# Kernel optimization log

Hardware: AMD Instinct MI355X
Metric: run time of the kernel (lower is better)

Reference implementation:

```python
import jax, jax.numpy as jnp
import numpy as np

EPS = 1.1920929e-07  # torch RMSNorm default eps = finfo(float32).eps
B, S, H, HQ, HKV, D, I, E, TOPK = 2, 512, 1024, 16, 4, 64, 4096, 8, 2


def rmsnorm(x, w):
    return x * jax.lax.rsqrt(jnp.mean(x * x, axis=-1, keepdims=True) + EPS) * w


def setup_inputs() -> dict:
    key = jax.random.key(0)
    ks = jax.random.split(key, 24)

    def w(k, shape, fan_in):
        return jax.random.normal(k, shape, jnp.float32) / np.float32(np.sqrt(fan_in))

    return {
        "x": jax.random.normal(ks[0], (B, S, H), jnp.float32),
        "norm1_w": jnp.ones((H,), jnp.float32),
        "q_w": w(ks[1], (H, HQ * D), H), "q_b": jnp.zeros((HQ * D,), jnp.float32),
        "k_w": w(ks[2], (H, HKV * D), H), "k_b": jnp.zeros((HKV * D,), jnp.float32),
        "v_w": w(ks[3], (H, HKV * D), H), "v_b": jnp.zeros((HKV * D,), jnp.float32),
        "o_w": w(ks[4], (HQ * D, H), HQ * D), "o_b": jnp.zeros((H,), jnp.float32),
        "norm2_w": jnp.ones((H,), jnp.float32),
        "router_w": w(ks[5], (H, E), H), "router_b": jnp.zeros((E,), jnp.float32),
        "gate_w": w(ks[6], (E, H, I), H), "gate_b": jnp.zeros((E, I), jnp.float32),
        "up_w": w(ks[7], (E, H, I), H), "up_b": jnp.zeros((E, I), jnp.float32),
        "down_w": w(ks[8], (E, I, H), I), "down_b": jnp.zeros((E, H), jnp.float32),
    }


def reference(x, norm1_w, q_w, q_b, k_w, k_b, v_w, v_b, o_w, o_b, norm2_w,
              router_w, router_b, gate_w, gate_b, up_w, up_b, down_w, down_b):
    # ---- self-attention (GQA, no mask, dropout=0) ----
    h = rmsnorm(x, norm1_w)
    q = (h @ q_w + q_b).reshape(B, S, HQ, D).transpose(0, 2, 1, 3)   # [B,HQ,S,D]
    k = (h @ k_w + k_b).reshape(B, S, HKV, D).transpose(0, 2, 1, 3)  # [B,HKV,S,D]
    v = (h @ v_w + v_b).reshape(B, S, HKV, D).transpose(0, 2, 1, 3)
    g = HQ // HKV
    k = jnp.repeat(k, g, axis=1)  # repeat_interleave, matches SDPA enable_gqa
    v = jnp.repeat(v, g, axis=1)
    scores = jnp.einsum('bhqd,bhkd->bhqk', q, k) * np.float32(1.0 / np.sqrt(D))
    attn = jax.nn.softmax(scores, axis=-1)
    o = jnp.einsum('bhqk,bhkd->bhqd', attn, v).transpose(0, 2, 1, 3).reshape(B, S, HQ * D)
    x = x + (o @ o_w + o_b)

    # ---- MoE (top-k routing, softmax over top-k logits) ----
    t = rmsnorm(x, norm2_w).reshape(B * S, H)                # [T,H]
    logits = t @ router_w + router_b                         # [T,E]
    top_v, top_i = jax.lax.top_k(logits, TOPK)
    probs = jax.nn.softmax(top_v, axis=-1)                   # [T,K]
    combine = jnp.einsum('tke,tk->te', jax.nn.one_hot(top_i, E, dtype=t.dtype), probs)  # [T,E]
    gt = jnp.einsum('th,ehi->tei', t, gate_w) + gate_b       # [T,E,I]
    up = jnp.einsum('th,ehi->tei', t, up_w) + up_b
    dn = jnp.einsum('tei,eih->teh', jax.nn.silu(gt) * up, down_w) + down_b  # [T,E,H]
    moe = jnp.einsum('teh,te->th', dn, combine).reshape(B, S, H)
    return moe + x
```

## Files before the change

kernel.cpp:

```cpp
#include <hip/hip_runtime.h>
#include <math.h>

#define T 1024
#define H 1024
#define S 512
#define BB 2
#define HQ 16
#define HKV 4
#define DH 64
#define NI 4096
#define NE 8
#define EPSR 1.1920929e-07f

typedef unsigned short u16;
using short8 = __attribute__((ext_vector_type(8))) short;
using f32x4  = __attribute__((ext_vector_type(4))) float;
using float4v = __attribute__((ext_vector_type(4))) float;

__device__ __forceinline__ float bf2f(u16 u) {
    unsigned int x = ((unsigned int)u) << 16;
    return __uint_as_float(x);
}
__device__ __forceinline__ u16 f2bf(float f) {
    unsigned int x = __float_as_uint(f);
    return (u16)((x + 0x7fffu + ((x >> 16) & 1u)) >> 16);
}

__global__ __launch_bounds__(256) void rmsnorm_k(const float* __restrict__ xin,
                                                 const float* __restrict__ w,
                                                 u16* __restrict__ out) {
    int t = blockIdx.x;
    int tid = threadIdx.x;
    float vals[4];
    float ss = 0.f;
#pragma unroll
    for (int i = 0; i < 4; i++) {
        int c = tid + i * 256;
        float v = xin[(long)t * H + c];
        vals[i] = v;
        ss += v * v;
    }
    int lane = tid & 63, wid = tid >> 6;
#pragma unroll
    for (int o = 32; o; o >>= 1) ss += __shfl_xor(ss, o);
    __shared__ float red[4];
    __shared__ float rtot;
    if (lane == 0) red[wid] = ss;
    __syncthreads();
    if (tid == 0) {
        float s = red[0] + red[1] + red[2] + red[3];
        rtot = rsqrtf(s / (float)H + EPSR);
    }
    __syncthreads();
    float r = rtot;
#pragma unroll
    for (int i = 0; i < 4; i++) {
        int c = tid + i * 256;
        out[(long)t * H + c] = f2bf(vals[i] * r * w[c]);
    }
}

template <int MODE>
__global__ __launch_bounds__(256) void gemm64(
    const u16* __restrict__ A, int lda,
    const float* __restrict__ B0, const float* __restrict__ B1, int ldb,
    const float* __restrict__ bias0, const float* __restrict__ bias1,
    const float* __restrict__ resid,
    void* __restrict__ out,
    int M, int N, int K,
    const int* __restrict__ ecnt, const int* __restrict__ eoff,
    const int* __restrict__ tlist, const float* __restrict__ tscale,
    u16* __restrict__ act, float* __restrict__ moe) {
    int e = blockIdx.z;
    int row0 = blockIdx.y * 64;
    int n0 = blockIdx.x * 64;
    int cnt = M, loff = 0;
    if (MODE >= 3) {
        cnt = ecnt[e];
        loff = eoff[e];
        if (row0 >= cnt) return;
        B0 += (long)e * (long)K * (long)ldb;
        bias0 += (long)e * N;
        if (MODE == 3) {
            B1 += (long)e * (long)K * (long)ldb;
            bias1 += (long)e * N;
        }
    }

    const int tid = threadIdx.x, lane = tid & 63, wv = tid >> 6;
    const int wm = wv >> 1, wc = wv & 1;

    __shared__ u16 As[64][40];
    __shared__ u16 Bs0[4][64][8];
    __shared__ u16 Bs1[(MODE == 3) ? 4 : 1][64][8];

    f32x4 acc0[2][2] = {};
    f32x4 acc1[2][2] = {};

    int arow = tid >> 2;
    int acol = (tid & 3) * 8;
    long arow_g;
    if (MODE == 3) {
        int r = row0 + arow;
        if (r >= cnt) r = cnt - 1;
        arow_g = tlist[loff + r];
    } else if (MODE == 4) {
        int r = row0 + arow;
        if (r >= cnt) r = cnt - 1;
        arow_g = loff + r;
    } else {
        arow_g = row0 + arow;
    }
    const u16* Aptr = A + arow_g * (long)lda + acol;

    int brow = tid >> 3;
    int bcol = (tid & 7) * 8;
    const float* B0ptr = B0 + (long)brow * ldb + n0 + bcol;
    const float* B1ptr = (MODE == 3) ? (B1 + (long)brow * ldb + n0 + bcol) : nullptr;

    for (int k0 = 0; k0 < K; k0 += 32) {
        short8 av = *(const short8*)(Aptr + k0);
        *(short8*)&As[arow][acol] = av;
        {
            float4v b0a = *(const float4v*)(B0ptr + (long)k0 * ldb);
            float4v b0b = *(const float4v*)(B0ptr + (long)k0 * ldb + 4);
#pragma unroll
            for (int u = 0; u < 4; u++) Bs0[brow >> 3][bcol + u][brow & 7] = f2bf(b0a[u]);
#pragma unroll
            for (int u = 0; u < 4; u++) Bs0[brow >> 3][bcol + 4 + u][brow & 7] = f2bf(b0b[u]);
        }
        if (MODE == 3) {
            float4v b1a = *(const float4v*)(B1ptr + (long)k0 * ldb);
            float4v b1b = *(const float4v*)(B1ptr + (long)k0 * ldb + 4);
#pragma unroll
            for (int u = 0; u < 4; u++) Bs1[brow >> 3][bcol + u][brow & 7] = f2bf(b1a[u]);
#pragma unroll
            for (int u = 0; u < 4; u++) Bs1[brow >> 3][bcol + 4 + u][brow & 7] = f2bf(b1b[u]);
        }
        __syncthreads();
        int quad = lane >> 4;
#pragma unroll
        for (int mi = 0; mi < 2; mi++) {
            int m = wm * 32 + mi * 16 + (lane & 15);
            short8 af = *(const short8*)&As[m][quad * 8];
#pragma unroll
            for (int ni = 0; ni < 2; ni++) {
                int n = wc * 32 + ni * 16 + (lane & 15);
                short8 bfr = *(const short8*)&Bs0[quad][n][0];
                acc0[mi][ni] = __builtin_amdgcn_mfma_f32_16x16x32_bf16(af, bfr, acc0[mi][ni], 0, 0, 0);
                if (MODE == 3) {
                    short8 bfu = *(const short8*)&Bs1[quad][n][0];
                    acc1[mi][ni] = __builtin_amdgcn_mfma_f32_16x16x32_bf16(af, bfu, acc1[mi][ni], 0, 0, 0);
                }
            }
        }
        __syncthreads();
    }

#pragma unroll
    for (int mi = 0; mi < 2; mi++) {
#pragma unroll
        for (int ni = 0; ni < 2; ni++) {
            int rbase = wm * 32 + mi * 16 + ((lane >> 4) << 2);
            int col = wc * 32 + ni * 16 + (lane & 15);
            int gcol = n0 + col;
#pragma unroll
            for (int r = 0; r < 4; r++) {
                int row = rbase + r;
                float v = acc0[mi][ni][r];
                if (MODE == 1) {
                    ((u16*)out)[(long)(row0 + row) * N + gcol] = f2bf(v + bias0[gcol]);
                } else if (MODE == 2) {
                    long idx = (long)(row0 + row) * N + gcol;
                    ((float*)out)[idx] = v + bias0[gcol] + resid[idx];
                } else if (MODE == 3) {
                    int rr = row0 + row;
                    if (rr < cnt) {
                        float g = v + bias0[gcol];
                        float u2 = acc1[mi][ni][r] + bias1[gcol];
                        float sg = g / (1.f + __expf(-g));
                        act[(long)(loff + rr) * NI + gcol] = f2bf(sg * u2);
                    }
                } else if (MODE == 4) {
                    int rr = row0 + row;
                    if (rr < cnt) {
                        int tok = tlist[loff + rr];
                        float sc = tscale[loff + rr];
                        atomicAdd(&moe[(long)tok * H + gcol], sc * (v + bias0[gcol]));
                    }
                }
            }
        }
    }
}

__global__ __launch_bounds__(256) void attn_k(const u16* __restrict__ q,
                                              const u16* __restrict__ k,
                                              const u16* __restrict__ v,
                                              u16* __restrict__ o) {
    int tid = threadIdx.x, lane = tid & 63, wv = tid >> 6;
    int w = blockIdx.x * 4 + wv;
    int sq = w % S;
    int h = (w / S) % HQ;
    int b = w / (S * HQ);
    int hk = h >> 2;
    int tq = b * S + sq;
    __shared__ float qs[4][64];
    __shared__ float ps[4][512];
    float* Q = qs[wv];
    float* P = ps[wv];
    Q[lane] = bf2f(q[(long)tq * (HQ * DH) + h * DH + lane]) * 0.125f;
    __syncthreads();
    float sc[8];
    float m = -1e30f;
#pragma unroll
    for (int jj = 0; jj < 8; jj++) {
        int j = lane + jj * 64;
        const u16* kr = k + (long)(b * S + j) * (HKV * DH) + hk * DH;
        float a = 0.f;
#pragma unroll
        for (int c = 0; c < 8; c++) {
            short8 kv8 = *(const short8*)(kr + c * 8);
#pragma unroll
            for (int u = 0; u < 8; u++) a += Q[c * 8 + u] * bf2f((u16)kv8[u]);
        }
        sc[jj] = a;
        m = fmaxf(m, a);
    }
#pragma unroll
    for (int o2 = 32; o2; o2 >>= 1) m = fmaxf(m, __shfl_xor(m, o2));
    float l = 0.f;
#pragma unroll
    for (int jj = 0; jj < 8; jj++) {
        float p = __expf(sc[jj] - m);
        P[lane + jj * 64] = p;
        l += p;
    }
#pragma unroll
    for (int o2 = 32; o2; o2 >>= 1) l += __shfl_xor(l, o2);
    __syncthreads();
    float inv = 1.f / l;
    float acc = 0.f;
    const u16* vb = v + (long)(b * S) * (HKV * DH) + hk * DH + lane;
#pragma unroll 4
    for (int j = 0; j < 512; j++) acc += P[j] * bf2f(vb[(long)j * (HKV * DH)]);
    o[(long)tq * (HQ * DH) + h * DH + lane] = f2bf(acc * inv);
}

__global__ __launch_bounds__(256) void router_k(const u16* __restrict__ t2,
                                                const float* __restrict__ rw,
                                                const float* __restrict__ rb,
                                                int* __restrict__ topi,
                                                float* __restrict__ probs) {
    int tid = threadIdx.x, lane = tid & 63, wv = tid >> 6;
    int tok = blockIdx.x * 4 + wv;
    float acc[NE] = {0.f, 0.f, 0.f, 0.f, 0.f, 0.f, 0.f, 0.f};
    for (int i = lane; i < H; i += 64) {
        float tv = bf2f(t2[(long)tok * H + i]);
        const float* r = rw + (long)i * NE;
        float4v ra = *(const float4v*)r;
        float4v rbv = *(const float4v*)(r + 4);
#pragma unroll
        for (int e = 0; e < 4; e++) acc[e] += tv * ra[e];
#pragma unroll
        for (int e = 0; e < 4; e++) acc[4 + e] += tv * rbv[e];
    }
#pragma unroll
    for (int e = 0; e < NE; e++)
#pragma unroll
        for (int o = 32; o; o >>= 1) acc[e] += __shfl_xor(acc[e], o);
    if (lane == 0) {
        float lg[NE];
#pragma unroll
        for (int e = 0; e < NE; e++) lg[e] = acc[e] + rb[e];
        int i0 = 0;
        float v0 = lg[0];
#pragma unroll
        for (int e = 1; e < NE; e++)
            if (lg[e] > v0) { v0 = lg[e]; i0 = e; }
        int i1 = -1;
        float v1 = -1e30f;
#pragma unroll
        for (int e = 0; e < NE; e++) {
            if (e == i0) continue;
            if (lg[e] > v1) { v1 = lg[e]; i1 = e; }
        }
        float ex = __expf(v1 - v0);
        float p0 = 1.f / (1.f + ex);
        topi[tok * 2] = i0;
        topi[tok * 2 + 1] = i1;
        probs[tok * 2] = p0;
        probs[tok * 2 + 1] = ex * p0;
    }
}

__global__ void build_k(const int* __restrict__ topi, const float* __restrict__ probs,
                        int* __restrict__ gcnt, int* __restrict__ goff,
                        int* __restrict__ list, float* __restrict__ lscale) {
    __shared__ int cnt[NE], off[NE], fill[NE];
    int t = threadIdx.x;
    if (t < NE) cnt[t] = 0;
    __syncthreads();
    int e0 = topi[2 * t], e1 = topi[2 * t + 1];
    atomicAdd(&cnt[e0], 1);
    atomicAdd(&cnt[e1], 1);
    __syncthreads();
    if (t == 0) {
        int run = 0;
        for (int e = 0; e < NE; e++) {
            off[e] = run;
            fill[e] = run;
            run += cnt[e];
        }
    }
    __syncthreads();
    if (t < NE) {
        gcnt[t] = cnt[t];
        goff[t] = off[t];
    }
    int p0 = atomicAdd(&fill[e0], 1);
    list[p0] = t;
    lscale[p0] = probs[2 * t];
    int p1 = atomicAdd(&fill[e1], 1);
    list[p1] = t;
    lscale[p1] = probs[2 * t + 1];
}

__global__ void zero_k(float* __restrict__ p, int n) {
    int i = blockIdx.x * 256 + threadIdx.x;
    if (i < n) p[i] = 0.f;
}

__global__ void final_k(const float* __restrict__ x1, const float* __restrict__ moe,
                        float* __restrict__ out) {
    int i = blockIdx.x * 256 + threadIdx.x;
    out[i] = x1[i] + moe[i];
}

extern "C" void kernel_launch(void* const* d_in, const int* in_sizes, int n_in,
                              void* d_out, int out_size, void* d_ws, size_t ws_size,
                              hipStream_t stream) {
    const float* x = (const float*)d_in[0];
    const float* norm1_w = (const float*)d_in[1];
    const float* q_w = (const float*)d_in[2];
    const float* q_b = (const float*)d_in[3];
    const float* k_w = (const float*)d_in[4];
    const float* k_b = (const float*)d_in[5];
    const float* v_w = (const float*)d_in[6];
    const float* v_b = (const float*)d_in[7];
    const float* o_w = (const float*)d_in[8];
    const float* o_b = (const float*)d_in[9];
    const float* norm2_w = (const float*)d_in[10];
    const float* router_w = (const float*)d_in[11];
    const float* router_b = (const float*)d_in[12];
    const float* gate_w = (const float*)d_in[13];
    const float* gate_b = (const float*)d_in[14];
    const float* up_w = (const float*)d_in[15];
    const float* up_b = (const float*)d_in[16];
    const float* down_w = (const float*)d_in[17];
    const float* down_b = (const float*)d_in[18];

    char* w = (char*)d_ws;
    u16* h1 = (u16*)w;            w += (long)T * H * 2;
    u16* qb = (u16*)w;            w += (long)T * (HQ * DH) * 2;
    u16* kb = (u16*)w;            w += (long)T * (HKV * DH) * 2;
    u16* vb = (u16*)w;            w += (long)T * (HKV * DH) * 2;
    u16* ao = (u16*)w;            w += (long)T * (HQ * DH) * 2;
    float* x1 = (float*)w;        w += (long)T * H * 4;
    u16* t2 = (u16*)w;            w += (long)T * H * 2;
    int* topi = (int*)w;          w += T * 2 * 4;
    float* probs = (float*)w;     w += T * 2 * 4;
    int* gcnt = (int*)w;          w += 64;
    int* goff = (int*)w;          w += 64;
    int* list = (int*)w;          w += 2048 * 4;
    float* lscale = (float*)w;    w += 2048 * 4;
    u16* act = (u16*)w;           w += (long)2112 * NI * 2;
    float* moe = (float*)w;       w += (long)T * H * 4;

    rmsnorm_k<<<T, 256, 0, stream>>>(x, norm1_w, h1);
    gemm64<1><<<dim3(16, 16, 1), 256, 0, stream>>>(h1, 1024, q_w, nullptr, 1024, q_b, nullptr,
                                                   nullptr, qb, 1024, 1024, 1024,
                                                   nullptr, nullptr, nullptr, nullptr, nullptr, nullptr);
    gemm64<1><<<dim3(4, 16, 1), 256, 0, stream>>>(h1, 1024, k_w, nullptr, 256, k_b, nullptr,
                                                  nullptr, kb, 1024, 256, 1024,
                                                  nullptr, nullptr, nullptr, nullptr, nullptr, nullptr);
    gemm64<1><<<dim3(4, 16, 1), 256, 0, stream>>>(h1, 1024, v_w, nullptr, 256, v_b, nullptr,
                                                  nullptr, vb, 1024, 256, 1024,
                                                  nullptr, nullptr, nullptr, nullptr, nullptr, nullptr);
    attn_k<<<(BB * HQ * S) / 4, 256, 0, stream>>>(qb, kb, vb, ao);
    gemm64<2><<<dim3(16, 16, 1), 256, 0, stream>>>(ao, 1024, o_w, nullptr, 1024, o_b, nullptr,
                                                   x, x1, 1024, 1024, 1024,
                                                   nullptr, nullptr, nullptr, nullptr, nullptr, nullptr);
    rmsnorm_k<<<T, 256, 0, stream>>>(x1, norm2_w, t2);
    router_k<<<T / 4, 256, 0, stream>>>(t2, router_w, router_b, topi, probs);
    build_k<<<1, 1024, 0, stream>>>(topi, probs, gcnt, goff, list, lscale);
    zero_k<<<(T * H) / 256, 256, 0, stream>>>(moe, T * H);
    gemm64<3><<<dim3(NI / 64, 16, NE), 256, 0, stream>>>(t2, 1024, gate_w, up_w, NI,
                                                         gate_b, up_b, nullptr, nullptr,
                                                         0, NI, 1024,
                                                         gcnt, goff, list, lscale, act, nullptr);
    gemm64<4><<<dim3(H / 64, 16, NE), 256, 0, stream>>>(act, NI, down_w, nullptr, H,
                                                        down_b, nullptr, nullptr, nullptr,
                                                        0, H, NI,
                                                        gcnt, goff, list, lscale, nullptr, moe);
    final_k<<<(T * H) / 256, 256, 0, stream>>>(x1, moe, (float*)d_out);
}
```

Measured before the change: 1.164 ms.

## Pre-transpose weights to bf16, enlarge GEMM tiles to 128, fuse QKV projection

Every weight matrix is first transposed and converted to bf16 by a dedicated kernel. The GEMM then loads K-contiguous bf16 rows with vector loads instead of converting fp32 inside the inner loop. GEMM tiles grow from 64x64 to 128x128 with a 4x4 MFMA block per wave, and the Q/K/V projections merge into one GEMM that writes a packed QKV buffer read by attention. The transposes run inside the timed call and rewrite about 200MB of expert weights on every call. The larger tiles also leave fewer blocks for the small routed expert batches.

```diff
diff --git a/kernel.cpp b/kernel.cpp
--- a/kernel.cpp
+++ b/kernel.cpp
@@ -26,6 +26,34 @@
     return (u16)((x + 0x7fffu + ((x >> 16) & 1u)) >> 16);
 }
 
+__global__ __launch_bounds__(256) void transpose_k(const float* __restrict__ W,
+                                                   u16* __restrict__ WT,
+                                                   int K, int N,
+                                                   long in_bs, long out_bs) {
+    int z = blockIdx.z;
+    W += z * in_bs;
+    WT += z * out_bs;
+    int n0 = blockIdx.x * 64, k0 = blockIdx.y * 64;
+    __shared__ u16 tile[64][68];
+    int t = threadIdx.x;
+    int r = t >> 4, c = (t & 15) * 4;
+#pragma unroll
+    for (int p = 0; p < 4; p++) {
+        float4v v = *(const float4v*)(W + (long)(k0 + r + p * 16) * N + n0 + c);
+#pragma unroll
+        for (int u = 0; u < 4; u++) tile[r + p * 16][c + u] = f2bf(v[u]);
+    }
+    __syncthreads();
+    int n = t >> 3, k8 = (t & 7) * 8;
+#pragma unroll
+    for (int p = 0; p < 2; p++) {
+        short8 o;
+#pragma unroll
+        for (int j = 0; j < 8; j++) o[j] = (short)tile[k8 + j][n + p * 32];
+        *(short8*)(WT + (long)(n0 + n + p * 32) * K + k0 + k8) = o;
+    }
+}
+
 __global__ __launch_bounds__(256) void rmsnorm_k(const float* __restrict__ xin,
                                                  const float* __restrict__ w,
                                                  u16* __restrict__ out) {
@@ -61,9 +89,9 @@
 }
 
 template <int MODE>
-__global__ __launch_bounds__(256) void gemm64(
+__global__ __launch_bounds__(256) void gemm128(
     const u16* __restrict__ A, int lda,
-    const float* __restrict__ B0, const float* __restrict__ B1, int ldb,
+    const u16* __restrict__ BT0, const u16* __restrict__ BT1,
     const float* __restrict__ bias0, const float* __restrict__ bias1,
     const float* __restrict__ resid,
     void* __restrict__ out,
@@ -72,98 +100,97 @@
     const int* __restrict__ tlist, const float* __restrict__ tscale,
     u16* __restrict__ act, float* __restrict__ moe) {
     int e = blockIdx.z;
-    int row0 = blockIdx.y * 64;
-    int n0 = blockIdx.x * 64;
+    int row0 = blockIdx.y * 128;
+    int n0 = blockIdx.x * 128;
     int cnt = M, loff = 0;
     if (MODE >= 3) {
         cnt = ecnt[e];
         loff = eoff[e];
         if (row0 >= cnt) return;
-        B0 += (long)e * (long)K * (long)ldb;
+        BT0 += (long)e * (long)K * (long)NI * ((MODE == 3) ? 1 : 0) + ((MODE == 4) ? (long)e * (long)K * (long)H : 0);
         bias0 += (long)e * N;
         if (MODE == 3) {
-            B1 += (long)e * (long)K * (long)ldb;
+            BT1 += (long)e * (long)K * (long)NI;
             bias1 += (long)e * N;
         }
     }
 
     const int tid = threadIdx.x, lane = tid & 63, wv = tid >> 6;
-    const int wm = wv >> 1, wc = wv & 1;
-
-    __shared__ u16 As[64][40];
-    __shared__ u16 Bs0[4][64][8];
-    __shared__ u16 Bs1[(MODE == 3) ? 4 : 1][64][8];
-
-    f32x4 acc0[2][2] = {};
-    f32x4 acc1[2][2] = {};
-
-    int arow = tid >> 2;
-    int acol = (tid & 3) * 8;
-    long arow_g;
-    if (MODE == 3) {
-        int r = row0 + arow;
-        if (r >= cnt) r = cnt - 1;
-        arow_g = tlist[loff + r];
-    } else if (MODE == 4) {
-        int r = row0 + arow;
-        if (r >= cnt) r = cnt - 1;
-        arow_g = loff + r;
-    } else {
-        arow_g = row0 + arow;
-    }
-    const u16* Aptr = A + arow_g * (long)lda + acol;
-
-    int brow = tid >> 3;
-    int bcol = (tid & 7) * 8;
-    const float* B0ptr = B0 + (long)brow * ldb + n0 + bcol;
-    const float* B1ptr = (MODE == 3) ? (B1 + (long)brow * ldb + n0 + bcol) : nullptr;
+    const int wm = wv >> 1, wn = wv & 1;
+    const int quad = lane >> 4, lm = lane & 15;
+
+    __shared__ u16 As[128][32];
+    __shared__ u16 Bs0[128][32];
+    __shared__ u16 Bs1[(MODE == 3) ? 128 : 1][32];
+
+    f32x4 acc0[4][4] = {};
+    f32x4 acc1[(MODE == 3) ? 4 : 1][4] = {};
+
+    int sa_row = tid >> 2;
+    int sa_k = (tid & 3) * 8;
+    long arow_g[2];
+#pragma unroll
+    for (int p = 0; p < 2; p++) {
+        int r = row0 + sa_row + p * 64;
+        if (MODE == 3) {
+            if (r >= cnt) r = row0 + ((cnt - 1 - row0) > 0 ? (cnt - 1 - row0) : 0);
+            int rr = (row0 + sa_row + p * 64 < cnt) ? (row0 + sa_row + p * 64) : (cnt - 1);
+            arow_g[p] = tlist[loff + rr];
+        } else if (MODE == 4) {
+            int rr = (r < cnt) ? r : (cnt - 1);
+            arow_g[p] = loff + rr;
+        } else {
+            arow_g[p] = r;
+        }
+    }
+    const u16* Ap0 = A + arow_g[0] * (long)lda + sa_k;
+    const u16* Ap1 = A + arow_g[1] * (long)lda + sa_k;
+    const u16* Bp0 = BT0 + (long)(n0 + sa_row) * K + sa_k;
+    const u16* Bp1 = BT0 + (long)(n0 + sa_row + 64) * K + sa_k;
+    const u16* Cp0 = (MODE == 3) ? (BT1 + (long)(n0 + sa_row) * K + sa_k) : nullptr;
+    const u16* Cp1 = (MODE == 3) ? (BT1 + (long)(n0 + sa_row + 64) * K + sa_k) : nullptr;
 
     for (int k0 = 0; k0 < K; k0 += 32) {
-        short8 av = *(const short8*)(Aptr + k0);
-        *(short8*)&As[arow][acol] = av;
-        {
-            float4v b0a = *(const float4v*)(B0ptr + (long)k0 * ldb);
-            float4v b0b = *(const float4v*)(B0ptr + (long)k0 * ldb + 4);
-#pragma unroll
-            for (int u = 0; u < 4; u++) Bs0[brow >> 3][bcol + u][brow & 7] = f2bf(b0a[u]);
-#pragma unroll
-            for (int u = 0; u < 4; u++) Bs0[brow >> 3][bcol + 4 + u][brow & 7] = f2bf(b0b[u]);
-        }
+        short8 a0 = *(const short8*)(Ap0 + k0);
+        short8 a1 = *(const short8*)(Ap1 + k0);
+        short8 b0 = *(const short8*)(Bp0 + k0);
+        short8 b1 = *(const short8*)(Bp1 + k0);
+        short8 c0, c1;
         if (MODE == 3) {
-            float4v b1a = *(const float4v*)(B1ptr + (long)k0 * ldb);
-            float4v b1b = *(const float4v*)(B1ptr + (long)k0 * ldb + 4);
-#pragma unroll
-            for (int u = 0; u < 4; u++) Bs1[brow >> 3][bcol + u][brow & 7] = f2bf(b1a[u]);
-#pragma unroll
-            for (int u = 0; u < 4; u++) Bs1[brow >> 3][bcol + 4 + u][brow & 7] = f2bf(b1b[u]);
+            c0 = *(const short8*)(Cp0 + k0);
+            c1 = *(const short8*)(Cp1 + k0);
         }
         __syncthreads();
-        int quad = lane >> 4;
-#pragma unroll
-        for (int mi = 0; mi < 2; mi++) {
-            int m = wm * 32 + mi * 16 + (lane & 15);
-            short8 af = *(const short8*)&As[m][quad * 8];
-#pragma unroll
-            for (int ni = 0; ni < 2; ni++) {
-                int n = wc * 32 + ni * 16 + (lane & 15);
-                short8 bfr = *(const short8*)&Bs0[quad][n][0];
-                acc0[mi][ni] = __builtin_amdgcn_mfma_f32_16x16x32_bf16(af, bfr, acc0[mi][ni], 0, 0, 0);
+        *(short8*)&As[sa_row][sa_k] = a0;
+        *(short8*)&As[sa_row + 64][sa_k] = a1;
+        *(short8*)&Bs0[sa_row][sa_k] = b0;
+        *(short8*)&Bs0[sa_row + 64][sa_k] = b1;
+        if (MODE == 3) {
+            *(short8*)&Bs1[sa_row][sa_k] = c0;
+            *(short8*)&Bs1[sa_row + 64][sa_k] = c1;
+        }
+        __syncthreads();
+#pragma unroll
+        for (int mi = 0; mi < 4; mi++) {
+            short8 af = *(const short8*)&As[wm * 64 + mi * 16 + lm][quad * 8];
+#pragma unroll
+            for (int ni = 0; ni < 4; ni++) {
+                short8 bf = *(const short8*)&Bs0[wn * 64 + ni * 16 + lm][quad * 8];
+                acc0[mi][ni] = __builtin_amdgcn_mfma_f32_16x16x32_bf16(af, bf, acc0[mi][ni], 0, 0, 0);
                 if (MODE == 3) {
-                    short8 bfu = *(const short8*)&Bs1[quad][n][0];
-                    acc1[mi][ni] = __builtin_amdgcn_mfma_f32_16x16x32_bf16(af, bfu, acc1[mi][ni], 0, 0, 0);
+                    short8 cf = *(const short8*)&Bs1[wn * 64 + ni * 16 + lm][quad * 8];
+                    acc1[mi][ni] = __builtin_amdgcn_mfma_f32_16x16x32_bf16(af, cf, acc1[mi][ni], 0, 0, 0);
                 }
             }
         }
-        __syncthreads();
-    }
-
-#pragma unroll
-    for (int mi = 0; mi < 2; mi++) {
-#pragma unroll
-        for (int ni = 0; ni < 2; ni++) {
-            int rbase = wm * 32 + mi * 16 + ((lane >> 4) << 2);
-            int col = wc * 32 + ni * 16 + (lane & 15);
-            int gcol = n0 + col;
+    }
+
+#pragma unroll
+    for (int mi = 0; mi < 4; mi++) {
+#pragma unroll
+        for (int ni = 0; ni < 4; ni++) {
+            int rbase = wm * 64 + mi * 16 + quad * 4;
+            int gcol = n0 + wn * 64 + ni * 16 + lm;
 #pragma unroll
             for (int r = 0; r < 4; r++) {
                 int row = rbase + r;
@@ -194,9 +221,8 @@
     }
 }
 
-__global__ __launch_bounds__(256) void attn_k(const u16* __restrict__ q,
-                                              const u16* __restrict__ k,
-                                              const u16* __restrict__ v,
+#define QKVLD 1536
+__global__ __launch_bounds__(256) void attn_k(const u16* __restrict__ qkv,
                                               u16* __restrict__ o) {
     int tid = threadIdx.x, lane = tid & 63, wv = tid >> 6;
     int w = blockIdx.x * 4 + wv;
@@ -209,14 +235,14 @@
     __shared__ float ps[4][512];
     float* Q = qs[wv];
     float* P = ps[wv];
-    Q[lane] = bf2f(q[(long)tq * (HQ * DH) + h * DH + lane]) * 0.125f;
+    Q[lane] = bf2f(qkv[(long)tq * QKVLD + h * DH + lane]) * 0.125f;
     __syncthreads();
     float sc[8];
     float m = -1e30f;
 #pragma unroll
     for (int jj = 0; jj < 8; jj++) {
         int j = lane + jj * 64;
-        const u16* kr = k + (long)(b * S + j) * (HKV * DH) + hk * DH;
+        const u16* kr = qkv + (long)(b * S + j) * QKVLD + 1024 + hk * DH;
         float a = 0.f;
 #pragma unroll
         for (int c = 0; c < 8; c++) {
@@ -241,9 +267,9 @@
     __syncthreads();
     float inv = 1.f / l;
     float acc = 0.f;
-    const u16* vb = v + (long)(b * S) * (HKV * DH) + hk * DH + lane;
+    const u16* vb = qkv + (long)(b * S) * QKVLD + 1280 + hk * DH + lane;
 #pragma unroll 4
-    for (int j = 0; j < 512; j++) acc += P[j] * bf2f(vb[(long)j * (HKV * DH)]);
+    for (int j = 0; j < 512; j++) acc += P[j] * bf2f(vb[(long)j * QKVLD]);
     o[(long)tq * (HQ * DH) + h * DH + lane] = f2bf(acc * inv);
 }
 
@@ -324,6 +350,15 @@
     int p1 = atomicAdd(&fill[e1], 1);
     list[p1] = t;
     lscale[p1] = probs[2 * t + 1];
+}
+
+__global__ void prep_bias_k(const float* __restrict__ qb, const float* __restrict__ kb,
+                            const float* __restrict__ vb, float* __restrict__ qkvb) {
+    int i = blockIdx.x * 256 + threadIdx.x;
+    if (i < 1536) {
+        float v = (i < 1024) ? qb[i] : ((i < 1280) ? kb[i - 1024] : vb[i - 1280]);
+        qkvb[i] = v;
+    }
 }
 
 __global__ void zero_k(float* __restrict__ p, int n) {
@@ -361,10 +396,14 @@
     const float* down_b = (const float*)d_in[18];
 
     char* w = (char*)d_ws;
+    u16* qkvT = (u16*)w;          w += (long)1536 * 1024 * 2;
+    u16* o_wt = (u16*)w;          w += (long)1024 * 1024 * 2;
+    u16* gateT = (u16*)w;         w += (long)NE * NI * 1024 * 2;
+    u16* upT = (u16*)w;           w += (long)NE * NI * 1024 * 2;
+    u16* downT = (u16*)w;         w += (long)NE * 1024 * NI * 2;
     u16* h1 = (u16*)w;            w += (long)T * H * 2;
-    u16* qb = (u16*)w;            w += (long)T * (HQ * DH) * 2;
-    u16* kb = (u16*)w;            w += (long)T * (HKV * DH) * 2;
-    u16* vb = (u16*)w;            w += (long)T * (HKV * DH) * 2;
+    u16* qkv = (u16*)w;           w += (long)T * 1536 * 2;
+    float* qkvb = (float*)w;      w += 1536 * 4;
     u16* ao = (u16*)w;            w += (long)T * (HQ * DH) * 2;
     float* x1 = (float*)w;        w += (long)T * H * 4;
     u16* t2 = (u16*)w;            w += (long)T * H * 2;
@@ -374,34 +413,40 @@
     int* goff = (int*)w;          w += 64;
     int* list = (int*)w;          w += 2048 * 4;
     float* lscale = (float*)w;    w += 2048 * 4;
-    u16* act = (u16*)w;           w += (long)2112 * NI * 2;
+    u16* act = (u16*)w;           w += (long)2048 * NI * 2;
     float* moe = (float*)w;       w += (long)T * H * 4;
 
+    transpose_k<<<dim3(16, 16, 1), 256, 0, stream>>>(q_w, qkvT, 1024, 1024, 0, 0);
+    transpose_k<<<dim3(4, 16, 1), 256, 0, stream>>>(k_w, qkvT + (long)1024 * 1024, 1024, 256, 0, 0);
+    transpose_k<<<dim3(4, 16, 1), 256, 0, stream>>>(v_w, qkvT + (long)1280 * 1024, 1024, 256, 0, 0);
+    transpose_k<<<dim3(16, 16, 1), 256, 0, stream>>>(o_w, o_wt, 1024, 1024, 0, 0);
+    transpose_k<<<dim3(64, 16, NE), 256, 0, stream>>>(gate_w, gateT, 1024, NI,
+                                                      (long)1024 * NI, (long)NI * 1024);
+    transpose_k<<<dim3(64, 16, NE), 256, 0, stream>>>(up_w, upT, 1024, NI,
+                                                      (long)1024 * NI, (long)NI * 1024);
+    transpose_k<<<dim3(16, 64, NE), 256, 0, stream>>>(down_w, downT, NI, 1024,
+                                                      (long)NI * 1024, (long)1024 * NI);
+    prep_bias_k<<<6, 256, 0, stream>>>(q_b, k_b, v_b, qkvb);
+
     rmsnorm_k<<<T, 256, 0, stream>>>(x, norm1_w, h1);
-    gemm64<1><<<dim3(16, 16, 1), 256, 0, stream>>>(h1, 1024, q_w, nullptr, 1024, q_b, nullptr,
-                                                   nullptr, qb, 1024, 1024, 1024,
+    gemm128<1><<<dim3(12, 8, 1), 256, 0, stream>>>(h1, 1024, qkvT, nullptr, qkvb, nullptr,
+                                                   nullptr, qkv, 1024, 1536, 1024,
                                                    nullptr, nullptr, nullptr, nullptr, nullptr, nullptr);
-    gemm64<1><<<dim3(4, 16, 1), 256, 0, stream>>>(h1, 1024, k_w, nullptr, 256, k_b, nullptr,
-                                                  nullptr, kb, 1024, 256, 1024,
+    attn_k<<<(BB * HQ * S) / 4, 256, 0, stream>>>(qkv, ao);
+    gemm128<2><<<dim3(8, 8, 1), 256, 0, stream>>>(ao, 1024, o_wt, nullptr, o_b, nullptr,
+                                                  x, x1, 1024, 1024, 1024,
                                                   nullptr, nullptr, nullptr, nullptr, nullptr, nullptr);
-    gemm64<1><<<dim3(4, 16, 1), 256, 0, stream>>>(h1, 1024, v_w, nullptr, 256, v_b, nullptr,
-                                                  nullptr, vb, 1024, 256, 1024,
-                                                  nullptr, nullptr, nullptr, nullptr, nullptr, nullptr);
-    attn_k<<<(BB * HQ * S) / 4, 256, 0, stream>>>(qb, kb, vb, ao);
-    gemm64<2><<<dim3(16, 16, 1), 256, 0, stream>>>(ao, 1024, o_w, nullptr, 1024, o_b, nullptr,
-                                                   x, x1, 1024, 1024, 1024,
-                                                   nullptr, nullptr, nullptr, nullptr, nullptr, nullptr);
     rmsnorm_k<<<T, 256, 0, stream>>>(x1, norm2_w, t2);
     router_k<<<T / 4, 256, 0, stream>>>(t2, router_w, router_b, topi, probs);
     build_k<<<1, 1024, 0, stream>>>(topi, probs, gcnt, goff, list, lscale);
     zero_k<<<(T * H) / 256, 256, 0, stream>>>(moe, T * H);
-    gemm64<3><<<dim3(NI / 64, 16, NE), 256, 0, stream>>>(t2, 1024, gate_w, up_w, NI,
-                                                         gate_b, up_b, nullptr, nullptr,
-                                                         0, NI, 1024,
-                                                         gcnt, goff, list, lscale, act, nullptr);
-    gemm64<4><<<dim3(H / 64, 16, NE), 256, 0, stream>>>(act, NI, down_w, nullptr, H,
-                                                        down_b, nullptr, nullptr, nullptr,
-                                                        0, H, NI,
-                                                        gcnt, goff, list, lscale, nullptr, moe);
+    gemm128<3><<<dim3(NI / 128, 8, NE), 256, 0, stream>>>(t2, 1024, gateT, upT,
+                                                          gate_b, up_b, nullptr, nullptr,
+                                                          0, NI, 1024,
+                                                          gcnt, goff, list, lscale, act, nullptr);
+    gemm128<4><<<dim3(H / 128, 8, NE), 256, 0, stream>>>(act, NI, downT, nullptr,
+                                                         down_b, nullptr, nullptr, nullptr,
+                                                         0, H, NI,
+                                                         gcnt, goff, list, lscale, nullptr, moe);
     final_k<<<(T * H) / 256, 256, 0, stream>>>(x1, moe, (float*)d_out);
 }
```

Result: faster. 1.064 ms (-8.6%).
